# Performance work log

Measured on AMD Instinct MI355X. Metric: run time of the kernel, lower is better.

## Reference

```python
import jax, jax.numpy as jnp
import numpy as np

B = 8
N_SRC = 2048   # coarse points per cloud
N_DST = 8192   # dense (skip) points per cloud
C_SRC = 128
C_SKIP = 64
K = 3
BN_EPS = 1e-5
LRELU_SLOPE = 0.01


def setup_inputs() -> dict:
    key = jax.random.key(0)
    ks = jax.random.split(key, 12)
    x = jax.random.normal(ks[0], (B * N_SRC, C_SRC), dtype=jnp.float32)
    pos = jax.random.normal(ks[1], (B * N_SRC, 3), dtype=jnp.float32)
    x_skip = jax.random.normal(ks[2], (B * N_DST, C_SKIP), dtype=jnp.float32)
    pos_skip = jax.random.normal(ks[3], (B * N_DST, 3), dtype=jnp.float32)
    batch = jnp.repeat(jnp.arange(B, dtype=jnp.int64), N_SRC)
    batch_skip = jnp.repeat(jnp.arange(B, dtype=jnp.int64), N_DST)
    c_in = C_SRC + C_SKIP  # 192
    c_h = 128
    # Linear weights: torch layout [out, in]
    W1 = jax.random.normal(ks[4], (c_h, c_in), dtype=jnp.float32) / np.sqrt(c_in)
    b1 = jax.random.normal(ks[5], (c_h,), dtype=jnp.float32) * 0.01
    g1 = jnp.ones((c_h,), dtype=jnp.float32)
    be1 = jnp.zeros((c_h,), dtype=jnp.float32)
    W2 = jax.random.normal(ks[6], (c_h, c_h), dtype=jnp.float32) / np.sqrt(c_h)
    b2 = jax.random.normal(ks[7], (c_h,), dtype=jnp.float32) * 0.01
    g2 = jnp.ones((c_h,), dtype=jnp.float32)
    be2 = jnp.zeros((c_h,), dtype=jnp.float32)
    return {"x": x, "pos": pos, "batch": batch, "x_skip": x_skip,
            "pos_skip": pos_skip, "batch_skip": batch_skip,
            "W1": W1, "b1": b1, "g1": g1, "be1": be1,
            "W2": W2, "b2": b2, "g2": g2, "be2": be2}


def _knn_interpolate(x, pos, pos_skip):
    # Uniform-sized batches -> reshape and process per cloud.
    xs = x.reshape(B, N_SRC, -1)          # [B, Ns, C]
    ps = pos.reshape(B, N_SRC, 3)
    pd = pos_skip.reshape(B, N_DST, 3)
    # Squared pairwise distances per cloud: [B, Nd, Ns]
    d2 = jnp.sum((pd[:, :, None, :] - ps[:, None, :, :]) ** 2, axis=-1)
    neg_d2, idx = jax.lax.top_k(-d2, K)   # k nearest -> [B, Nd, K]
    w = 1.0 / jnp.maximum(-neg_d2, 1e-16)  # inverse squared distance weights
    feats = jax.vmap(lambda f, i: f[i])(xs, idx)  # [B, Nd, K, C]
    y = jnp.sum(w[..., None] * feats, axis=2) / jnp.sum(w, axis=2, keepdims=True)
    return y.reshape(B * N_DST, -1)


def _mlp_block(h, W, b, g, be):
    h = h @ W.T + b
    h = jnp.where(h > 0, h, LRELU_SLOPE * h)  # LeakyReLU
    mean = jnp.mean(h, axis=0)
    var = jnp.mean((h - mean) ** 2, axis=0)   # biased var (BN training mode)
    h = (h - mean) * jax.lax.rsqrt(var + BN_EPS)
    return h * g + be


def reference(x, pos, batch, x_skip, pos_skip, batch_skip,
              W1, b1, g1, be1, W2, b2, g2, be2):
    h = _knn_interpolate(x, pos, pos_skip)      # [B*Nd, C_SRC]
    h = jnp.concatenate([h, x_skip], axis=1)    # [B*Nd, C_SRC+C_SKIP]
    h = _mlp_block(h, W1, b1, g1, be1)
    h = _mlp_block(h, W2, b2, g2, be2)
    return (h, pos_skip, batch_skip)
```

## Files before the change

kernel.cpp:

```cpp
#include <hip/hip_runtime.h>
#include <math.h>

#define NB 8
#define N_SRC 2048
#define N_DST 8192
#define C_SRC 128
#define C_SKIP 64
#define C_IN 192
#define C_H 128
#define N_ROWS (NB * N_DST)
#define BN_EPS 1e-5f
#define SLOPE 0.01f
#define GEMM_BLOCKS (N_ROWS / 64)

using short8 = __attribute__((ext_vector_type(8))) short;
using f32x4  = __attribute__((ext_vector_type(4))) float;
using sf16   = __attribute__((ext_vector_type(16))) float;

static __device__ __forceinline__ unsigned short f2bf(float f) {
    unsigned u = __builtin_bit_cast(unsigned, f);
    u = u + 0x7FFFu + ((u >> 16) & 1u);
    return (unsigned short)(u >> 16);
}
static __device__ __forceinline__ float bflo(unsigned v) {
    return __builtin_bit_cast(float, (v & 0xFFFFu) << 16);
}
static __device__ __forceinline__ float bfhi(unsigned v) {
    return __builtin_bit_cast(float, v & 0xFFFF0000u);
}

__global__ __launch_bounds__(256) void k_prep(const float* __restrict__ W1,
                                              unsigned short* __restrict__ W1bf,
                                              const float* __restrict__ W2,
                                              unsigned short* __restrict__ W2bf,
                                              const float* __restrict__ pos,
                                              float4* __restrict__ pos4,
                                              const float* __restrict__ pos_skip,
                                              const int* __restrict__ batch_skip,
                                              float* __restrict__ out_pos,
                                              float* __restrict__ out_batch) {
    int gid = blockIdx.x * 256 + threadIdx.x;
    int stride = gridDim.x * 256;
    for (int i = gid; i < C_H * C_IN; i += stride) W1bf[i] = f2bf(W1[i]);
    for (int i = gid; i < C_H * C_H; i += stride)  W2bf[i] = f2bf(W2[i]);
    for (int p = gid; p < NB * N_SRC; p += stride) {
        pos4[p] = make_float4(pos[p * 3 + 0], pos[p * 3 + 1], pos[p * 3 + 2], 0.f);
    }
    for (int i = gid; i < N_ROWS * 3 / 4; i += stride) {
        ((float4*)out_pos)[i] = ((const float4*)pos_skip)[i];
    }
    for (int i = gid; i < N_ROWS; i += stride) {
        out_batch[i] = (float)batch_skip[i];
    }
}

__global__ __launch_bounds__(512, 8) void k_fused1(
    const float4* __restrict__ pos4, const float* __restrict__ pos_skip,
    const float* __restrict__ x, const float* __restrict__ x_skip,
    const unsigned short* __restrict__ Wbf, const float* __restrict__ bias,
    float* __restrict__ out, unsigned short* __restrict__ h1bf,
    float* __restrict__ ps, float* __restrict__ pq) {
    __shared__ __align__(16) unsigned short Ash[64][200];
    __shared__ float sS[4][128];
    __shared__ float sQ[4][128];
    __shared__ int   midx[64][3];
    __shared__ float mw[64][3];

    float* cd = (float*)&Ash[0][0];
    int*   ci = (int*)((char*)&Ash[0][0] + 6144);

    int tid = threadIdx.x;
    int l = tid & 63;
    int v = __builtin_amdgcn_readfirstlane(tid >> 6);
    int blk = blockIdx.x;
    int cloud = blk & 7;
    int tile  = blk >> 3;
    int r0 = cloud * N_DST + tile * 64;

    int dst = r0 + l;
    float px = pos_skip[dst * 3 + 0];
    float py = pos_skip[dst * 3 + 1];
    float pz = pos_skip[dst * 3 + 2];

    float rr0 = 3.4e38f, rr1 = 3.4e38f, rr2 = 3.4e38f;
    int   ii0 = 0, ii1 = 0, ii2 = 0;

    const char* sp = (const char*)(pos4 + (cloud << 11) + (v << 8));
    for (int g = 0; g < 32; ++g) {
        sf16 A, B;
        asm volatile("s_load_dwordx16 %0, %2, 0x0\n\t"
                     "s_load_dwordx16 %1, %2, 0x40\n\t"
                     "s_waitcnt lgkmcnt(0)"
                     : "=s"(A), "=s"(B)
                     : "s"(sp));
        sp += 128;
        int jb = (v << 8) + g * 8;
#pragma unroll
        for (int k = 0; k < 4; ++k) {
            float dx = px - A[4 * k], dy = py - A[4 * k + 1], dz = pz - A[4 * k + 2];
            float d = fmaf(dx, dx, fmaf(dy, dy, dz * dz));
            if (d < rr2) {
                int jj = jb + k;
                bool c0 = d < rr0, c1 = d < rr1;
                ii2 = c1 ? ii1 : jj;              rr2 = c1 ? rr1 : d;
                ii1 = c1 ? (c0 ? ii0 : jj) : ii1; rr1 = c1 ? (c0 ? rr0 : d) : rr1;
                ii0 = c0 ? jj : ii0;              rr0 = c0 ? d : rr0;
            }
        }
#pragma unroll
        for (int k = 0; k < 4; ++k) {
            float dx = px - B[4 * k], dy = py - B[4 * k + 1], dz = pz - B[4 * k + 2];
            float d = fmaf(dx, dx, fmaf(dy, dy, dz * dz));
            if (d < rr2) {
                int jj = jb + 4 + k;
                bool c0 = d < rr0, c1 = d < rr1;
                ii2 = c1 ? ii1 : jj;              rr2 = c1 ? rr1 : d;
                ii1 = c1 ? (c0 ? ii0 : jj) : ii1; rr1 = c1 ? (c0 ? rr0 : d) : rr1;
                ii0 = c0 ? jj : ii0;              rr0 = c0 ? d : rr0;
            }
        }
    }
    cd[(v * 64 + l) * 3 + 0] = rr0; ci[(v * 64 + l) * 3 + 0] = ii0;
    cd[(v * 64 + l) * 3 + 1] = rr1; ci[(v * 64 + l) * 3 + 1] = ii1;
    cd[(v * 64 + l) * 3 + 2] = rr2; ci[(v * 64 + l) * 3 + 2] = ii2;
    __syncthreads();

    if (tid < 64) {
        float e0 = 3.4e38f, e1 = 3.4e38f, e2 = 3.4e38f;
        int   m0 = 0, m1 = 0, m2 = 0;
#pragma unroll
        for (int s = 0; s < 8; ++s) {
#pragma unroll
            for (int t = 0; t < 3; ++t) {
                float d = cd[(s * 64 + tid) * 3 + t];
                int  jj = ci[(s * 64 + tid) * 3 + t];
                if (d < e2) {
                    bool c0 = d < e0, c1 = d < e1;
                    m2 = c1 ? m1 : jj;            e2 = c1 ? e1 : d;
                    m1 = c1 ? (c0 ? m0 : jj) : m1; e1 = c1 ? (c0 ? e0 : d) : e1;
                    m0 = c0 ? jj : m0;            e0 = c0 ? d : e0;
                }
            }
        }
        float w0 = 1.f / fmaxf(e0, 1e-16f);
        float w1 = 1.f / fmaxf(e1, 1e-16f);
        float w2 = 1.f / fmaxf(e2, 1e-16f);
        float inv = 1.f / (w0 + w1 + w2);
        midx[tid][0] = m0; midx[tid][1] = m1; midx[tid][2] = m2;
        mw[tid][0] = w0 * inv; mw[tid][1] = w1 * inv; mw[tid][2] = w2 * inv;
    }
    __syncthreads();

    const float* xb = x + (size_t)cloud * N_SRC * C_SRC;
    for (int rr = v * 8; rr < v * 8 + 8; ++rr) {
        int j0 = midx[rr][0], j1 = midx[rr][1], j2 = midx[rr][2];
        float w0 = mw[rr][0], w1 = mw[rr][1], w2 = mw[rr][2];
        const float2* x0v = (const float2*)(xb + (size_t)j0 * C_SRC);
        const float2* x1v = (const float2*)(xb + (size_t)j1 * C_SRC);
        const float2* x2v = (const float2*)(xb + (size_t)j2 * C_SRC);
        float2 a = x0v[l], b = x1v[l], c = x2v[l];
        float v0 = w0 * a.x + w1 * b.x + w2 * c.x;
        float v1 = w0 * a.y + w1 * b.y + w2 * c.y;
        ((unsigned*)&Ash[rr][0])[l] = (unsigned)f2bf(v0) | ((unsigned)f2bf(v1) << 16);
        Ash[rr][128 + l] = f2bf(x_skip[(size_t)(r0 + rr) * C_SKIP + l]);
    }
    __syncthreads();

    int wr = v & 3, wc = v >> 2;
    int cl = l & 15, kh = l >> 4;
    f32x4 acc[4];
#pragma unroll
    for (int n = 0; n < 4; ++n) {
        float bv = bias[wc * 64 + n * 16 + cl];
        acc[n][0] = bv; acc[n][1] = bv; acc[n][2] = bv; acc[n][3] = bv;
    }
    const unsigned short* wb = Wbf + (size_t)(wc * 4) * 16 * C_IN +
                               (size_t)cl * C_IN + kh * 8;
    for (int kt = 0; kt < 6; ++kt) {
        short8 af = *(const short8*)&Ash[wr * 16 + cl][kt * 32 + kh * 8];
#pragma unroll
        for (int n = 0; n < 4; ++n) {
            short8 bf = *(const short8*)(wb + (size_t)n * 16 * C_IN + kt * 32);
            acc[n] = __builtin_amdgcn_mfma_f32_16x16x32_bf16(af, bf, acc[n], 0, 0, 0);
        }
    }

    float pss[4], pqs[4];
#pragma unroll
    for (int n = 0; n < 4; ++n) {
        float s = 0.f, q = 0.f;
#pragma unroll
        for (int j = 0; j < 4; ++j) {
            float z = acc[n][j];
            z = z > 0.f ? z : SLOPE * z;
            acc[n][j] = z;
            s += z; q += z * z;
        }
        s += __shfl_xor(s, 16); s += __shfl_xor(s, 32);
        q += __shfl_xor(q, 16); q += __shfl_xor(q, 32);
        pss[n] = s; pqs[n] = q;
    }

    __syncthreads();
    if (l < 16) {
#pragma unroll
        for (int n = 0; n < 4; ++n) {
            sS[wr][wc * 64 + n * 16 + l] = pss[n];
            sQ[wr][wc * 64 + n * 16 + l] = pqs[n];
        }
    }
    if (h1bf) {
        unsigned short* Az = (unsigned short*)&Ash[0][0];
#pragma unroll
        for (int n = 0; n < 4; ++n) {
            int col = wc * 64 + n * 16 + cl;
#pragma unroll
            for (int j = 0; j < 4; ++j) {
                Az[(wr * 16 + kh * 4 + j) * 128 + col] = f2bf(acc[n][j]);
            }
        }
    } else {
#pragma unroll
        for (int n = 0; n < 4; ++n) {
            int col = wc * 64 + n * 16 + cl;
#pragma unroll
            for (int j = 0; j < 4; ++j) {
                out[(size_t)(r0 + wr * 16 + kh * 4 + j) * C_H + col] = acc[n][j];
            }
        }
    }
    __syncthreads();
    if (h1bf) {
        const uint4* Asrc = (const uint4*)&Ash[0][0];
        uint4* zdst = (uint4*)(h1bf + (size_t)r0 * C_H);
        for (int i = tid; i < 64 * C_H / 8; i += 512) zdst[i] = Asrc[i];
    }
    if (tid < 128) {
        float s = sS[0][tid] + sS[1][tid] + sS[2][tid] + sS[3][tid];
        float q = sQ[0][tid] + sQ[1][tid] + sQ[2][tid] + sQ[3][tid];
        ps[blk * C_H + tid] = s;
        pq[blk * C_H + tid] = q;
    }
}

__global__ __launch_bounds__(256) void k_reduce(const float* __restrict__ ps,
                                                const float* __restrict__ pq,
                                                const float* __restrict__ g,
                                                const float* __restrict__ be,
                                                float* __restrict__ a_out,
                                                float* __restrict__ c_out) {
    int col = blockIdx.x;
    float s = 0.f, q = 0.f;
    for (int b = threadIdx.x; b < GEMM_BLOCKS; b += 256) {
        s += ps[b * C_H + col];
        q += pq[b * C_H + col];
    }
    for (int off = 32; off; off >>= 1) {
        s += __shfl_down(s, off);
        q += __shfl_down(q, off);
    }
    __shared__ float rs[4], rq[4];
    if ((threadIdx.x & 63) == 0) { rs[threadIdx.x >> 6] = s; rq[threadIdx.x >> 6] = q; }
    __syncthreads();
    if (threadIdx.x == 0) {
        s = rs[0] + rs[1] + rs[2] + rs[3];
        q = rq[0] + rq[1] + rq[2] + rq[3];
        float mean = s / (float)N_ROWS;
        float var  = q / (float)N_ROWS - mean * mean;
        float a = g[col] * rsqrtf(var + BN_EPS);
        a_out[col] = a;
        c_out[col] = be[col] - mean * a;
    }
}

__global__ __launch_bounds__(256) void k_g2a(const float* __restrict__ h,
                                             unsigned short* __restrict__ h1bf,
                                             const unsigned short* __restrict__ Wbf,
                                             const float* __restrict__ b2,
                                             const float* __restrict__ a1,
                                             const float* __restrict__ c1,
                                             float* __restrict__ ps,
                                             float* __restrict__ pq) {
    __shared__ __align__(16) unsigned short Ash[64][136];
    __shared__ float sS[4][128];
    __shared__ float sQ[4][128];

    int r0 = blockIdx.x * 64;
    int tid = threadIdx.x;
    int l = tid & 63, w = tid >> 6;

    if (h1bf) {
        const uint4* src = (const uint4*)(h1bf + (size_t)r0 * C_H);
        for (int i = tid; i < 64 * C_H / 8; i += 256) {
            uint4 vv = src[i];
            int c0 = (i * 8) & 127, r = (i * 8) >> 7;
            float4 a0 = *(const float4*)&a1[c0];
            float4 a4 = *(const float4*)&a1[c0 + 4];
            float4 c0v = *(const float4*)&c1[c0];
            float4 c4v = *(const float4*)&c1[c0 + 4];
            unsigned o0 = (unsigned)f2bf(fmaf(a0.x, bflo(vv.x), c0v.x)) |
                          ((unsigned)f2bf(fmaf(a0.y, bfhi(vv.x), c0v.y)) << 16);
            unsigned o1 = (unsigned)f2bf(fmaf(a0.z, bflo(vv.y), c0v.z)) |
                          ((unsigned)f2bf(fmaf(a0.w, bfhi(vv.y), c0v.w)) << 16);
            unsigned o2 = (unsigned)f2bf(fmaf(a4.x, bflo(vv.z), c4v.x)) |
                          ((unsigned)f2bf(fmaf(a4.y, bfhi(vv.z), c4v.y)) << 16);
            unsigned o3 = (unsigned)f2bf(fmaf(a4.z, bflo(vv.w), c4v.z)) |
                          ((unsigned)f2bf(fmaf(a4.w, bfhi(vv.w), c4v.w)) << 16);
            *(uint4*)&Ash[r][c0] = make_uint4(o0, o1, o2, o3);
        }
    } else {
        const float* src = h + (size_t)r0 * C_H;
        for (int i = tid * 4; i < 64 * C_H; i += 1024) {
            float4 vf = *(const float4*)&src[i];
            int r = i >> 7, c = i & 127;
            float4 av = *(const float4*)&a1[c];
            float4 cv = *(const float4*)&c1[c];
            unsigned lo = (unsigned)f2bf(fmaf(av.x, vf.x, cv.x)) |
                          ((unsigned)f2bf(fmaf(av.y, vf.y, cv.y)) << 16);
            unsigned hi = (unsigned)f2bf(fmaf(av.z, vf.z, cv.z)) |
                          ((unsigned)f2bf(fmaf(av.w, vf.w, cv.w)) << 16);
            *(uint2*)&Ash[r][c] = make_uint2(lo, hi);
        }
    }
    __syncthreads();

    int cl = l & 15, kh = l >> 4;
    f32x4 acc[8];
#pragma unroll
    for (int n = 0; n < 8; ++n) {
        float bv = b2[n * 16 + cl];
        acc[n][0] = bv; acc[n][1] = bv; acc[n][2] = bv; acc[n][3] = bv;
    }
    const unsigned short* wb = Wbf + (size_t)cl * C_H + kh * 8;
    for (int kt = 0; kt < 4; ++kt) {
        short8 af = *(const short8*)&Ash[w * 16 + cl][kt * 32 + kh * 8];
#pragma unroll
        for (int n = 0; n < 8; ++n) {
            short8 bf = *(const short8*)(wb + (size_t)n * 16 * C_H + kt * 32);
            acc[n] = __builtin_amdgcn_mfma_f32_16x16x32_bf16(af, bf, acc[n], 0, 0, 0);
        }
    }

    float pss[8], pqs[8];
#pragma unroll
    for (int n = 0; n < 8; ++n) {
        float s = 0.f, q = 0.f;
#pragma unroll
        for (int j = 0; j < 4; ++j) {
            float z = acc[n][j];
            z = z > 0.f ? z : SLOPE * z;
            acc[n][j] = z;
            s += z; q += z * z;
        }
        s += __shfl_xor(s, 16); s += __shfl_xor(s, 32);
        q += __shfl_xor(q, 16); q += __shfl_xor(q, 32);
        pss[n] = s; pqs[n] = q;
    }

    if (h1bf) {
        __syncthreads();
        unsigned short* Az = (unsigned short*)&Ash[0][0];
#pragma unroll
        for (int n = 0; n < 8; ++n) {
            int col = n * 16 + cl;
#pragma unroll
            for (int j = 0; j < 4; ++j) {
                Az[(w * 16 + kh * 4 + j) * 128 + col] = f2bf(acc[n][j]);
            }
        }
    }
    if (l < 16) {
#pragma unroll
        for (int n = 0; n < 8; ++n) {
            sS[w][n * 16 + l] = pss[n];
            sQ[w][n * 16 + l] = pqs[n];
        }
    }
    __syncthreads();
    if (h1bf) {
        const uint4* Asrc = (const uint4*)&Ash[0][0];
        uint4* zdst = (uint4*)(h1bf + (size_t)r0 * C_H);
        for (int i = tid; i < 64 * C_H / 8; i += 256) zdst[i] = Asrc[i];
    }
    if (tid < 128) {
        float s = sS[0][tid] + sS[1][tid] + sS[2][tid] + sS[3][tid];
        float q = sQ[0][tid] + sQ[1][tid] + sQ[2][tid] + sQ[3][tid];
        ps[blockIdx.x * C_H + tid] = s;
        pq[blockIdx.x * C_H + tid] = q;
    }
}

__global__ __launch_bounds__(256) void k_final(const unsigned short* __restrict__ z2bf,
                                               const float* __restrict__ a2,
                                               const float* __restrict__ c2,
                                               float* __restrict__ out_h) {
    __shared__ float sa[128], sc[128];
    int tid = threadIdx.x;
    if (tid < 128) { sa[tid] = a2[tid]; sc[tid] = c2[tid]; }
    __syncthreads();

    int gid = blockIdx.x * 256 + tid;
    int stride = gridDim.x * 256;
    const uint4* zsrc = (const uint4*)z2bf;
    for (int i = gid; i < N_ROWS * C_H / 8; i += stride) {
        uint4 v = zsrc[i];
        int c0 = (i * 8) & 127;
        float4 o0, o1;
        o0.x = fmaf(sa[c0 + 0], bflo(v.x), sc[c0 + 0]);
        o0.y = fmaf(sa[c0 + 1], bfhi(v.x), sc[c0 + 1]);
        o0.z = fmaf(sa[c0 + 2], bflo(v.y), sc[c0 + 2]);
        o0.w = fmaf(sa[c0 + 3], bfhi(v.y), sc[c0 + 3]);
        o1.x = fmaf(sa[c0 + 4], bflo(v.z), sc[c0 + 4]);
        o1.y = fmaf(sa[c0 + 5], bfhi(v.z), sc[c0 + 5]);
        o1.z = fmaf(sa[c0 + 6], bflo(v.w), sc[c0 + 6]);
        o1.w = fmaf(sa[c0 + 7], bfhi(v.w), sc[c0 + 7]);
        *(float4*)&out_h[(size_t)i * 8]     = o0;
        *(float4*)&out_h[(size_t)i * 8 + 4] = o1;
    }
}

__global__ __launch_bounds__(256) void k_g2b(float* __restrict__ h,
                                             const unsigned short* __restrict__ Wbf,
                                             const float* __restrict__ b2,
                                             const float* __restrict__ a1,
                                             const float* __restrict__ c1,
                                             const float* __restrict__ a2,
                                             const float* __restrict__ c2) {
    __shared__ __align__(16) unsigned short Ash[64][136];

    int r0 = blockIdx.x * 64;
    int tid = threadIdx.x;
    int l = tid & 63, w = tid >> 6;

    const float* src = h + (size_t)r0 * C_H;
    for (int i = tid * 4; i < 64 * C_H; i += 1024) {
        float4 vf = *(const float4*)&src[i];
        int r = i >> 7, c = i & 127;
        float4 av = *(const float4*)&a1[c];
        float4 cv = *(const float4*)&c1[c];
        unsigned lo = (unsigned)f2bf(fmaf(av.x, vf.x, cv.x)) |
                      ((unsigned)f2bf(fmaf(av.y, vf.y, cv.y)) << 16);
        unsigned hi = (unsigned)f2bf(fmaf(av.z, vf.z, cv.z)) |
                      ((unsigned)f2bf(fmaf(av.w, vf.w, cv.w)) << 16);
        *(uint2*)&Ash[r][c] = make_uint2(lo, hi);
    }
    __syncthreads();

    int cl = l & 15, kh = l >> 4;
    f32x4 acc[8];
#pragma unroll
    for (int n = 0; n < 8; ++n) {
        float bv = b2[n * 16 + cl];
        acc[n][0] = bv; acc[n][1] = bv; acc[n][2] = bv; acc[n][3] = bv;
    }
    const unsigned short* wb = Wbf + (size_t)cl * C_H + kh * 8;
    for (int kt = 0; kt < 4; ++kt) {
        short8 af = *(const short8*)&Ash[w * 16 + cl][kt * 32 + kh * 8];
#pragma unroll
        for (int n = 0; n < 8; ++n) {
            short8 bf = *(const short8*)(wb + (size_t)n * 16 * C_H + kt * 32);
            acc[n] = __builtin_amdgcn_mfma_f32_16x16x32_bf16(af, bf, acc[n], 0, 0, 0);
        }
    }

#pragma unroll
    for (int n = 0; n < 8; ++n) {
        int col = n * 16 + cl;
        float av = a2[col], cv = c2[col];
#pragma unroll
        for (int j = 0; j < 4; ++j) {
            int row = r0 + w * 16 + kh * 4 + j;
            float z = acc[n][j];
            z = z > 0.f ? z : SLOPE * z;
            h[(size_t)row * C_H + col] = av * z + cv;
        }
    }
}

extern "C" void kernel_launch(void* const* d_in, const int* in_sizes, int n_in,
                              void* d_out, int out_size, void* d_ws, size_t ws_size,
                              hipStream_t stream) {
    const float* x          = (const float*)d_in[0];
    const float* pos        = (const float*)d_in[1];
    const float* x_skip     = (const float*)d_in[3];
    const float* pos_skip   = (const float*)d_in[4];
    const int*   batch_skip = (const int*)d_in[5];
    const float* W1  = (const float*)d_in[6];
    const float* b1  = (const float*)d_in[7];
    const float* g1  = (const float*)d_in[8];
    const float* be1 = (const float*)d_in[9];
    const float* W2  = (const float*)d_in[10];
    const float* b2  = (const float*)d_in[11];
    const float* g2  = (const float*)d_in[12];
    const float* be2 = (const float*)d_in[13];

    float* out_h     = (float*)d_out;
    float* out_pos   = out_h + (size_t)N_ROWS * C_H;
    float* out_batch = out_pos + (size_t)N_ROWS * 3;

    float* wsf = (float*)d_ws;
    float4* pos4         = (float4*)wsf;
    unsigned short* W1bf = (unsigned short*)(wsf + 65536);
    unsigned short* W2bf = (unsigned short*)(wsf + 77824);
    float* p1s = wsf + 86016;
    float* p1q = p1s + 131072;
    float* p2s = p1q + 131072;
    float* p2q = p2s + 131072;
    float* a1g = p2q + 131072;
    float* c1g = a1g + 128;
    float* a2g = c1g + 128;
    float* c2g = a2g + 128;
    unsigned short* zbuf = (unsigned short*)(c2g + 128);
    size_t ws_needed = ((size_t)610816 * 4) + (size_t)N_ROWS * C_H * 2;
    bool use_z = ws_size >= ws_needed;
    unsigned short* h1bf = use_z ? zbuf : (unsigned short*)nullptr;

    k_prep<<<256, 256, 0, stream>>>(W1, W1bf, W2, W2bf, pos, pos4,
                                    pos_skip, batch_skip, out_pos, out_batch);
    k_fused1<<<GEMM_BLOCKS, 512, 0, stream>>>(pos4, pos_skip, x, x_skip, W1bf, b1,
                                              out_h, h1bf, p1s, p1q);
    k_reduce<<<C_H, 256, 0, stream>>>(p1s, p1q, g1, be1, a1g, c1g);
    k_g2a<<<GEMM_BLOCKS, 256, 0, stream>>>(out_h, h1bf, W2bf, b2, a1g, c1g,
                                           p2s, p2q);
    k_reduce<<<C_H, 256, 0, stream>>>(p2s, p2q, g2, be2, a2g, c2g);
    if (use_z) {
        k_final<<<1024, 256, 0, stream>>>(zbuf, a2g, c2g, out_h);
    } else {
        k_g2b<<<GEMM_BLOCKS, 256, 0, stream>>>(out_h, W2bf, b2, a1g, c1g, a2g, c2g);
    }
}
```

Baseline: 112.9 us.

## Split kNN into distance-only med3 pass and index-recovery rescan

Replaces the branchy top-3 insertion that tracks both distances and indices with a branchless med3/min sort over distances only. After the three nearest distances are merged across waves, the kernel rescans all source points and writes the index of each point whose distance matches a threshold slot into shared memory. This removes the divergent branches and index selects from the hot loop, but recomputes every distance a second time. Ties or equal distances can make several lanes write the same slot, so the recovered indices may differ from the original tie-breaking.

```diff
diff --git a/kernel.cpp b/kernel.cpp
--- a/kernel.cpp
+++ b/kernel.cpp
@@ -67,7 +67,7 @@
     __shared__ float mw[64][3];
 
     float* cd = (float*)&Ash[0][0];
-    int*   ci = (int*)((char*)&Ash[0][0] + 6144);
+    float* eD = (float*)((char*)&Ash[0][0] + 6144);
 
     int tid = threadIdx.x;
     int l = tid & 63;
@@ -82,72 +82,95 @@
     float py = pos_skip[dst * 3 + 1];
     float pz = pos_skip[dst * 3 + 2];
 
-    float rr0 = 3.4e38f, rr1 = 3.4e38f, rr2 = 3.4e38f;
-    int   ii0 = 0, ii1 = 0, ii2 = 0;
-
-    const char* sp = (const char*)(pos4 + (cloud << 11) + (v << 8));
-    for (int g = 0; g < 32; ++g) {
-        sf16 A, B;
-        asm volatile("s_load_dwordx16 %0, %2, 0x0\n\t"
-                     "s_load_dwordx16 %1, %2, 0x40\n\t"
-                     "s_waitcnt lgkmcnt(0)"
-                     : "=s"(A), "=s"(B)
-                     : "s"(sp));
-        sp += 128;
-        int jb = (v << 8) + g * 8;
-#pragma unroll
-        for (int k = 0; k < 4; ++k) {
-            float dx = px - A[4 * k], dy = py - A[4 * k + 1], dz = pz - A[4 * k + 2];
-            float d = fmaf(dx, dx, fmaf(dy, dy, dz * dz));
-            if (d < rr2) {
-                int jj = jb + k;
-                bool c0 = d < rr0, c1 = d < rr1;
-                ii2 = c1 ? ii1 : jj;              rr2 = c1 ? rr1 : d;
-                ii1 = c1 ? (c0 ? ii0 : jj) : ii1; rr1 = c1 ? (c0 ? rr0 : d) : rr1;
-                ii0 = c0 ? jj : ii0;              rr0 = c0 ? d : rr0;
-            }
-        }
-#pragma unroll
-        for (int k = 0; k < 4; ++k) {
-            float dx = px - B[4 * k], dy = py - B[4 * k + 1], dz = pz - B[4 * k + 2];
-            float d = fmaf(dx, dx, fmaf(dy, dy, dz * dz));
-            if (d < rr2) {
-                int jj = jb + 4 + k;
-                bool c0 = d < rr0, c1 = d < rr1;
-                ii2 = c1 ? ii1 : jj;              rr2 = c1 ? rr1 : d;
-                ii1 = c1 ? (c0 ? ii0 : jj) : ii1; rr1 = c1 ? (c0 ? rr0 : d) : rr1;
-                ii0 = c0 ? jj : ii0;              rr0 = c0 ? d : rr0;
-            }
-        }
-    }
-    cd[(v * 64 + l) * 3 + 0] = rr0; ci[(v * 64 + l) * 3 + 0] = ii0;
-    cd[(v * 64 + l) * 3 + 1] = rr1; ci[(v * 64 + l) * 3 + 1] = ii1;
-    cd[(v * 64 + l) * 3 + 2] = rr2; ci[(v * 64 + l) * 3 + 2] = ii2;
+    float d0 = 3.4e38f, d1 = 3.4e38f, d2 = 3.4e38f;
+    {
+        const char* sp = (const char*)(pos4 + (cloud << 11) + (v << 8));
+        for (int g = 0; g < 32; ++g) {
+            sf16 A, B;
+            asm volatile("s_load_dwordx16 %0, %2, 0x0\n\t"
+                         "s_load_dwordx16 %1, %2, 0x40\n\t"
+                         "s_waitcnt lgkmcnt(0)"
+                         : "=s"(A), "=s"(B)
+                         : "s"(sp));
+            sp += 128;
+#pragma unroll
+            for (int k = 0; k < 4; ++k) {
+                float dx = px - A[4 * k], dy = py - A[4 * k + 1], dz = pz - A[4 * k + 2];
+                float d = fmaf(dx, dx, fmaf(dy, dy, dz * dz));
+                d2 = __builtin_amdgcn_fmed3f(d, d1, d2);
+                d1 = __builtin_amdgcn_fmed3f(d, d0, d1);
+                d0 = fminf(d0, d);
+            }
+#pragma unroll
+            for (int k = 0; k < 4; ++k) {
+                float dx = px - B[4 * k], dy = py - B[4 * k + 1], dz = pz - B[4 * k + 2];
+                float d = fmaf(dx, dx, fmaf(dy, dy, dz * dz));
+                d2 = __builtin_amdgcn_fmed3f(d, d1, d2);
+                d1 = __builtin_amdgcn_fmed3f(d, d0, d1);
+                d0 = fminf(d0, d);
+            }
+        }
+    }
+    cd[(v * 64 + l) * 3 + 0] = d0;
+    cd[(v * 64 + l) * 3 + 1] = d1;
+    cd[(v * 64 + l) * 3 + 2] = d2;
     __syncthreads();
 
     if (tid < 64) {
         float e0 = 3.4e38f, e1 = 3.4e38f, e2 = 3.4e38f;
-        int   m0 = 0, m1 = 0, m2 = 0;
 #pragma unroll
         for (int s = 0; s < 8; ++s) {
 #pragma unroll
             for (int t = 0; t < 3; ++t) {
                 float d = cd[(s * 64 + tid) * 3 + t];
-                int  jj = ci[(s * 64 + tid) * 3 + t];
-                if (d < e2) {
-                    bool c0 = d < e0, c1 = d < e1;
-                    m2 = c1 ? m1 : jj;            e2 = c1 ? e1 : d;
-                    m1 = c1 ? (c0 ? m0 : jj) : m1; e1 = c1 ? (c0 ? e0 : d) : e1;
-                    m0 = c0 ? jj : m0;            e0 = c0 ? d : e0;
-                }
+                e2 = __builtin_amdgcn_fmed3f(d, e1, e2);
+                e1 = __builtin_amdgcn_fmed3f(d, e0, e1);
+                e0 = fminf(e0, d);
             }
         }
         float w0 = 1.f / fmaxf(e0, 1e-16f);
         float w1 = 1.f / fmaxf(e1, 1e-16f);
         float w2 = 1.f / fmaxf(e2, 1e-16f);
         float inv = 1.f / (w0 + w1 + w2);
-        midx[tid][0] = m0; midx[tid][1] = m1; midx[tid][2] = m2;
         mw[tid][0] = w0 * inv; mw[tid][1] = w1 * inv; mw[tid][2] = w2 * inv;
+        eD[tid * 3 + 0] = e0; eD[tid * 3 + 1] = e1; eD[tid * 3 + 2] = e2;
+        midx[tid][0] = 0; midx[tid][1] = 0; midx[tid][2] = 0;
+    }
+    __syncthreads();
+
+    {
+        float e0r = eD[l * 3 + 0];
+        float e1r = eD[l * 3 + 1];
+        float e2r = eD[l * 3 + 2];
+        const char* sp = (const char*)(pos4 + (cloud << 11) + (v << 8));
+        for (int g = 0; g < 32; ++g) {
+            sf16 A, B;
+            asm volatile("s_load_dwordx16 %0, %2, 0x0\n\t"
+                         "s_load_dwordx16 %1, %2, 0x40\n\t"
+                         "s_waitcnt lgkmcnt(0)"
+                         : "=s"(A), "=s"(B)
+                         : "s"(sp));
+            sp += 128;
+            int jb = (v << 8) + g * 8;
+#pragma unroll
+            for (int k = 0; k < 4; ++k) {
+                float dx = px - A[4 * k], dy = py - A[4 * k + 1], dz = pz - A[4 * k + 2];
+                float d = fmaf(dx, dx, fmaf(dy, dy, dz * dz));
+                if (d <= e2r) {
+                    int slot = d <= e0r ? 0 : (d <= e1r ? 1 : 2);
+                    midx[l][slot] = jb + k;
+                }
+            }
+#pragma unroll
+            for (int k = 0; k < 4; ++k) {
+                float dx = px - B[4 * k], dy = py - B[4 * k + 1], dz = pz - B[4 * k + 2];
+                float d = fmaf(dx, dx, fmaf(dy, dy, dz * dz));
+                if (d <= e2r) {
+                    int slot = d <= e0r ? 0 : (d <= e1r ? 1 : 2);
+                    midx[l][slot] = jb + 4 + k;
+                }
+            }
+        }
     }
     __syncthreads();
 
```

Result: no change. 111.4 us (-1.3%).
